# Kernel optimization log

Measured on AMD Instinct MI355X. Metric: run time of the kernel, lower is better.

The kernel has to match this reference:

```python
import jax, jax.numpy as jnp
import numpy as np

NUM_GRAPHS = 256
NODES_PER_GRAPH = 64
K = 24
HID = 128

elu = jax.nn.elu


def _knn_edge_conv(x, Wc, bc):
    # x: [B*N, D]. Recompute kNN graph per graph, edge MLP, max-aggregate.
    B, N = NUM_GRAPHS, NODES_PER_GRAPH
    xg = x.reshape(B, N, -1)                       # [B, N, D]
    sq = jnp.sum(xg * xg, axis=-1)                 # [B, N]
    # squared euclidean distances within each graph: [B, N, N]
    d = sq[:, :, None] + sq[:, None, :] - 2.0 * jnp.einsum('bnd,bmd->bnm', xg, xg)
    _, idx = jax.lax.top_k(-d, K)                  # [B, N, K] nearest (incl. self)
    xj = jax.vmap(lambda g, i: g[i])(xg, idx)      # [B, N, K, D] neighbor gather
    xi = xg[:, :, None, :]                         # [B, N, 1, D]
    e = jnp.concatenate([jnp.broadcast_to(xi, xj.shape), xj - xi], axis=-1)  # [B,N,K,2D]
    m = elu(jnp.einsum('bnkf,fh->bnkh', e, Wc) + bc)
    out = jnp.max(m, axis=2)                       # max aggregation over K neighbors
    return out.reshape(B * N, -1)


def setup_inputs() -> dict:
    key = jax.random.key(0)
    ks = jax.random.split(key, 16)
    Ntot = NUM_GRAPHS * NODES_PER_GRAPH

    def w(k, fan_in, fan_out):
        return jax.random.normal(k, (fan_in, fan_out), jnp.float32) / np.sqrt(fan_in)

    return {
        'x_pf': jax.random.normal(ks[0], (Ntot, 15), jnp.float32),
        'batch_pf': jnp.repeat(jnp.arange(NUM_GRAPHS, dtype=jnp.int64 if jax.config.jax_enable_x64 else jnp.int32), NODES_PER_GRAPH),
        'W1': w(ks[1], 15, HID),  'b1': jnp.zeros((HID,), jnp.float32),
        'W2': w(ks[2], HID, HID), 'b2': jnp.zeros((HID,), jnp.float32),
        'Wc': w(ks[3], 2 * HID, HID), 'bc': jnp.zeros((HID,), jnp.float32),
        'Wo1': w(ks[4], HID, 64), 'bo1': jnp.zeros((64,), jnp.float32),
        'Wo2': w(ks[5], 64, 32),  'bo2': jnp.zeros((32,), jnp.float32),
        'Wo3': w(ks[6], 32, 32),  'bo3': jnp.zeros((32,), jnp.float32),
        'Wo4': w(ks[7], 32, 8),   'bo4': jnp.zeros((8,), jnp.float32),
    }


def reference(x_pf, batch_pf, W1, b1, W2, b2, Wc, bc, Wo1, bo1, Wo2, bo2, Wo3, bo3, Wo4, bo4):
    # pf_encode: Linear(15,128)+ELU+Linear(128,128)+ELU
    h = elu(elu(x_pf @ W1 + b1) @ W2 + b2)
    f1 = _knn_edge_conv(h, Wc, bc)
    f2 = _knn_edge_conv(f1, Wc, bc)
    f3 = _knn_edge_conv(f2, Wc, bc)
    # global_add_pool over nodes per graph
    pooled = jax.ops.segment_sum(f3, batch_pf, num_segments=NUM_GRAPHS)  # [B, 128]
    o = elu(pooled @ Wo1 + bo1)
    o = elu(o @ Wo2 + bo2)
    o = elu(o @ Wo3 + bo3)
    out = o @ Wo4 + bo4  # [B, 8]
    return (out, batch_pf)
```

## Files before the change

### kernel.cpp

```cpp
#include <hip/hip_runtime.h>
#include <hip/hip_bf16.h>
#include <math.h>

#define NG  256
#define NN  64
#define KK  24
#define HID 128
#define KP  136
#define FP  132
#define DP  68
#define FRAG 512
#define SLAB (8*4*2*FRAG)
#define HSLAB (8*4*FRAG)
#define IMG_BYTES (3*SLAB*2)

typedef __attribute__((ext_vector_type(8)))  short bf16x8;
typedef __attribute__((ext_vector_type(4)))  float f32x4;

__device__ __forceinline__ float elu1(float x){ return x > 0.f ? x : (expf(x)-1.f); }

__device__ __forceinline__ short bf_t(float x){ return (short)(__float_as_uint(x) >> 16); }
__device__ __forceinline__ float bf_u(short s){ return __uint_as_float(((unsigned)(unsigned short)s) << 16); }

extern "C" __global__ void prep_kernel(const float* __restrict__ W2,
                                       const float* __restrict__ Wc,
                                       short* __restrict__ img)
{
    int t = blockIdx.x * 256 + threadIdx.x;
    if (t >= 3*8*4*64) return;
    const int lane = t & 63;
    const int ks   = (t >> 6) & 3;
    const int tn   = (t >> 8) & 7;
    const int s    = t >> 11;
    const int n     = tn*16 + (lane & 15);
    const int kbase = ks*32 + (lane >> 4)*8;
    bf16x8 hv, lv;
    #pragma unroll
    for (int j = 0; j < 8; ++j){
        const int k = kbase + j;
        float w = (s == 0) ? W2[k*HID + n]
                : (s == 1) ? Wc[k*HID + n]
                           : Wc[(k + HID)*HID + n];
        short h = bf_t(w);
        hv[j] = h;
        lv[j] = bf_t(w - bf_u(h));
    }
    short* dst = img + s*SLAB + ((tn*4 + ks)*2)*FRAG + lane*8;
    *(bf16x8*)(dst)        = hv;
    *(bf16x8*)(dst + FRAG) = lv;
}

__device__ __forceinline__ void stage_copy(const short* __restrict__ src,
                                           short* __restrict__ slab, int tid)
{
    const uint4* s = (const uint4*)src;
    uint4* d = (uint4*)slab;
    #pragma unroll
    for (int i = 0; i < 4; ++i) d[tid + i*1024] = s[tid + i*1024];
}

__device__ __forceinline__ void stage_build(const float* __restrict__ Wg, int rowoff,
                                            short* __restrict__ slab, int tid)
{
    for (int i = tid; i < 8*4*64; i += 1024){
        const int lane2 = i & 63;
        const int ks    = (i >> 6) & 3;
        const int tn    = (i >> 8) & 7;
        const int n     = tn*16 + (lane2 & 15);
        const int kbase = ks*32 + (lane2 >> 4)*8;
        bf16x8 hv, lv;
        #pragma unroll
        for (int j = 0; j < 8; ++j){
            float w = Wg[(rowoff + kbase + j)*HID + n];
            short h = bf_t(w);
            hv[j] = h;
            lv[j] = bf_t(w - bf_u(h));
        }
        short* dst = slab + ((tn*4 + ks)*2)*FRAG + lane2*8;
        *(bf16x8*)(dst)        = hv;
        *(bf16x8*)(dst + FRAG) = lv;
    }
}

__device__ __forceinline__ void stage_hi_uv(const short* __restrict__ img,
                                            short* __restrict__ uv, int tid)
{
    const uint4* s = (const uint4*)img;
    uint4* d = (uint4*)uv;
    #pragma unroll
    for (int k = 0; k < 4; ++k){
        const int idx    = tid + k*1024;
        const int sl     = idx >> 11;
        const int within = idx & 2047;
        const int f      = within >> 6;
        const int w      = within & 63;
        d[idx] = s[(1 + sl)*4096 + f*128 + w];
    }
}

__device__ __forceinline__ void build_hi_uv(const float* __restrict__ Wc,
                                            short* __restrict__ uv, int tid)
{
    #pragma unroll
    for (int k = 0; k < 4; ++k){
        const int idx    = tid + k*1024;
        const int sl     = idx >> 11;
        const int within = idx & 2047;
        const int f      = within >> 6;
        const int lane2  = within & 63;
        const int tn = f >> 2, ks = f & 3;
        const int n     = tn*16 + (lane2 & 15);
        const int kbase = ks*32 + (lane2 >> 4)*8;
        const int rowoff = sl ? HID : 0;
        bf16x8 hv;
        #pragma unroll
        for (int j = 0; j < 8; ++j) hv[j] = bf_t(Wc[(rowoff + kbase + j)*HID + n]);
        *(bf16x8*)(uv + (size_t)idx*8) = hv;
    }
}

__device__ __forceinline__ void gemm16x2(const short* __restrict__ fbhi,
                                         const short* __restrict__ fblo,
                                         const short* __restrict__ slab,
                                         int tm, int tn0, int tn1, int lane,
                                         f32x4& c0, f32x4& c1)
{
    const int arow = tm*16 + (lane & 15);
    const int ko   = (lane >> 4) * 8;
    #pragma unroll 2
    for (int ks = 0; ks < 4; ++ks){
        bf16x8 ah = *(const bf16x8*)(fbhi + arow*KP + ks*32 + ko);
        bf16x8 al = *(const bf16x8*)(fblo + arow*KP + ks*32 + ko);
        const short* p0 = slab + ((tn0*4 + ks)*2)*FRAG + lane*8;
        const short* p1 = slab + ((tn1*4 + ks)*2)*FRAG + lane*8;
        bf16x8 bh0 = *(const bf16x8*)(p0);
        bf16x8 bl0 = *(const bf16x8*)(p0 + FRAG);
        bf16x8 bh1 = *(const bf16x8*)(p1);
        bf16x8 bl1 = *(const bf16x8*)(p1 + FRAG);
        c0 = __builtin_amdgcn_mfma_f32_16x16x32_bf16(ah, bh0, c0, 0,0,0);
        c0 = __builtin_amdgcn_mfma_f32_16x16x32_bf16(ah, bl0, c0, 0,0,0);
        c0 = __builtin_amdgcn_mfma_f32_16x16x32_bf16(al, bh0, c0, 0,0,0);
        c1 = __builtin_amdgcn_mfma_f32_16x16x32_bf16(ah, bh1, c1, 0,0,0);
        c1 = __builtin_amdgcn_mfma_f32_16x16x32_bf16(ah, bl1, c1, 0,0,0);
        c1 = __builtin_amdgcn_mfma_f32_16x16x32_bf16(al, bh1, c1, 0,0,0);
    }
}

extern "C" __global__ void __launch_bounds__(1024)
dgcnn_kernel(const float* __restrict__ x_pf,
             const float* __restrict__ W1, const float* __restrict__ b1,
             const float* __restrict__ W2, const float* __restrict__ b2,
             const float* __restrict__ Wc, const float* __restrict__ bc,
             const float* __restrict__ Wo1, const float* __restrict__ bo1,
             const float* __restrict__ Wo2, const float* __restrict__ bo2,
             const float* __restrict__ Wo3, const float* __restrict__ bo3,
             const float* __restrict__ Wo4, const float* __restrict__ bo4,
             const short* __restrict__ img, int use_img,
             float* __restrict__ out)
{
    __shared__ __align__(16) short fbhi[NN*KP];
    __shared__ __align__(16) short fblo[NN*KP];
    __shared__ __align__(16) float dmt[NN*DP];
    __shared__ __align__(16) float Vbuf[NN*FP];
    __shared__ __align__(16) short wslab[SLAB];
    __shared__ int   knn[NN*KK];
    __shared__ float sq[NN];

    const int tid  = threadIdx.x;
    const int g    = blockIdx.x;
    const int lane = tid & 63;
    const int wv   = tid >> 6;
    const int row1 = tid >> 4;
    const int c0i  = (tid & 15) * 8;
    const int c2   = (tid & 15) * 4;

    const int t0  = wv*2, t1 = wv*2 + 1;
    const int gtm = t0 >> 3;
    const int gtn0 = t0 & 7, gtn1 = t1 & 7;

    if (tid < NN) out[NG*8 + g*NN + tid] = (float)g;

    if (use_img) stage_copy(img + 0*SLAB, wslab, tid); else stage_build(W2, 0, wslab, tid);

    {
        float acc[8];
        {
            float4 bA = *(const float4*)(b1 + c0i);
            float4 bB = *(const float4*)(b1 + c0i + 4);
            acc[0]=bA.x; acc[1]=bA.y; acc[2]=bA.z; acc[3]=bA.w;
            acc[4]=bB.x; acc[5]=bB.y; acc[6]=bB.z; acc[7]=bB.w;
        }
        #pragma unroll
        for (int f = 0; f < 15; ++f){
            float xv = x_pf[g*NN*15 + row1*15 + f];
            float4 wA = *(const float4*)(W1 + f*HID + c0i);
            float4 wB = *(const float4*)(W1 + f*HID + c0i + 4);
            acc[0] += xv*wA.x; acc[1] += xv*wA.y; acc[2] += xv*wA.z; acc[3] += xv*wA.w;
            acc[4] += xv*wB.x; acc[5] += xv*wB.y; acc[6] += xv*wB.z; acc[7] += xv*wB.w;
        }
        short4 hA, lA, hB, lB;
        float v;
        v = elu1(acc[0]); hA.x = bf_t(v); lA.x = bf_t(v - bf_u(hA.x));
        v = elu1(acc[1]); hA.y = bf_t(v); lA.y = bf_t(v - bf_u(hA.y));
        v = elu1(acc[2]); hA.z = bf_t(v); lA.z = bf_t(v - bf_u(hA.z));
        v = elu1(acc[3]); hA.w = bf_t(v); lA.w = bf_t(v - bf_u(hA.w));
        v = elu1(acc[4]); hB.x = bf_t(v); lB.x = bf_t(v - bf_u(hB.x));
        v = elu1(acc[5]); hB.y = bf_t(v); lB.y = bf_t(v - bf_u(hB.y));
        v = elu1(acc[6]); hB.z = bf_t(v); lB.z = bf_t(v - bf_u(hB.z));
        v = elu1(acc[7]); hB.w = bf_t(v); lB.w = bf_t(v - bf_u(hB.w));
        *(short4*)(fbhi + row1*KP + c0i)     = hA;
        *(short4*)(fbhi + row1*KP + c0i + 4) = hB;
        *(short4*)(fblo + row1*KP + c0i)     = lA;
        *(short4*)(fblo + row1*KP + c0i + 4) = lB;
    }
    __syncthreads();

    {
        f32x4 cA = {0,0,0,0}, cB = {0,0,0,0};
        gemm16x2(fbhi, fblo, wslab, gtm, gtn0, gtn1, lane, cA, cB);
        __syncthreads();
        #pragma unroll
        for (int half = 0; half < 2; ++half){
            const int tn  = half ? gtn1 : gtn0;
            const f32x4 c = half ? cB : cA;
            const int col = tn*16 + (lane & 15);
            const int rb  = gtm*16 + (lane >> 4)*4;
            const float bb = b2[col];
            #pragma unroll
            for (int e = 0; e < 4; ++e){
                float vv = elu1(c[e] + bb);
                short h = bf_t(vv);
                fbhi[(rb + e)*KP + col] = h;
                fblo[(rb + e)*KP + col] = bf_t(vv - bf_u(h));
            }
        }
        if (use_img) stage_hi_uv(img, wslab, tid); else build_hi_uv(Wc, wslab, tid);
    }
    __syncthreads();

    {
        bf16x8 hv = *(const bf16x8*)(fbhi + row1*KP + c0i);
        bf16x8 lv = *(const bf16x8*)(fblo + row1*KP + c0i);
        float s = 0.f;
        #pragma unroll
        for (int j = 0; j < 8; ++j){
            float vv = bf_u(hv[j]) + bf_u(lv[j]);
            s += vv*vv;
        }
        s += __shfl_xor(s, 1, 64);
        s += __shfl_xor(s, 2, 64);
        s += __shfl_xor(s, 4, 64);
        s += __shfl_xor(s, 8, 64);
        if ((tid & 15) == 0) sq[row1] = s;
    }
    __syncthreads();

    const short* Uhi = wslab;
    const short* Vhi = wslab + HSLAB;

    for (int layer = 0; layer < 3; ++layer){
        f32x4 uA = {0,0,0,0}, uB = {0,0,0,0}, vA = {0,0,0,0}, vB = {0,0,0,0};
        {
            f32x4 dc = {0.f, 0.f, 0.f, 0.f};
            const int tm0 = wv >> 2, tn0d = wv & 3;
            const int arow = tm0*16 + (lane & 15);
            const int rB   = tn0d*16 + (lane & 15);
            const int ko   = (lane >> 4) * 8;
            #pragma unroll
            for (int ks = 0; ks < 4; ++ks){
                bf16x8 ah = *(const bf16x8*)(fbhi + arow*KP + ks*32 + ko);
                bf16x8 al = *(const bf16x8*)(fblo + arow*KP + ks*32 + ko);
                bf16x8 bh = *(const bf16x8*)(fbhi + rB*KP + ks*32 + ko);
                bf16x8 bl = *(const bf16x8*)(fblo + rB*KP + ks*32 + ko);
                dc = __builtin_amdgcn_mfma_f32_16x16x32_bf16(ah, bh, dc, 0,0,0);
                dc = __builtin_amdgcn_mfma_f32_16x16x32_bf16(ah, bl, dc, 0,0,0);
                dc = __builtin_amdgcn_mfma_f32_16x16x32_bf16(al, bh, dc, 0,0,0);
                const int f0 = (gtn0*4 + ks)*FRAG + lane*8;
                const int f1 = (gtn1*4 + ks)*FRAG + lane*8;
                bf16x8 bu0 = *(const bf16x8*)(Uhi + f0);
                bf16x8 bu1 = *(const bf16x8*)(Uhi + f1);
                bf16x8 bv0 = *(const bf16x8*)(Vhi + f0);
                bf16x8 bv1 = *(const bf16x8*)(Vhi + f1);
                uA = __builtin_amdgcn_mfma_f32_16x16x32_bf16(ah, bu0, uA, 0,0,0);
                uA = __builtin_amdgcn_mfma_f32_16x16x32_bf16(al, bu0, uA, 0,0,0);
                uB = __builtin_amdgcn_mfma_f32_16x16x32_bf16(ah, bu1, uB, 0,0,0);
                uB = __builtin_amdgcn_mfma_f32_16x16x32_bf16(al, bu1, uB, 0,0,0);
                vA = __builtin_amdgcn_mfma_f32_16x16x32_bf16(ah, bv0, vA, 0,0,0);
                vA = __builtin_amdgcn_mfma_f32_16x16x32_bf16(al, bv0, vA, 0,0,0);
                vB = __builtin_amdgcn_mfma_f32_16x16x32_bf16(ah, bv1, vB, 0,0,0);
                vB = __builtin_amdgcn_mfma_f32_16x16x32_bf16(al, bv1, vB, 0,0,0);
            }
            #pragma unroll
            for (int e = 0; e < 4; ++e){
                const int ra = tm0*16 + (lane >> 4)*4 + e, ca = tn0d*16 + (lane & 15);
                dmt[ra*DP + ca] = sq[ra] + sq[ca] - 2.f*dc[e];
            }
        }
        __syncthreads();

        {
            #pragma unroll
            for (int half = 0; half < 2; ++half){
                const int tn  = half ? gtn1 : gtn0;
                const f32x4 cv = half ? vB : vA;
                const f32x4 cu = half ? uB : uA;
                const int col = tn*16 + (lane & 15);
                const int rb  = gtm*16 + (lane >> 4)*4;
                #pragma unroll
                for (int e = 0; e < 4; ++e){
                    Vbuf[(rb + e)*FP + col] = cv[e];
                    float u = cu[e];
                    short h = bf_t(u);
                    fbhi[(rb + e)*KP + col] = h;
                    fblo[(rb + e)*KP + col] = bf_t(u - bf_u(h));
                }
            }
            #pragma unroll
            for (int p = 0; p < 4; ++p){
                const int r = wv*4 + p;
                const float dm = dmt[r*DP + lane];
                int rank = 0;
                #pragma unroll 4
                for (int q = 0; q < 16; ++q){
                    float4 v = *(const float4*)(dmt + r*DP + q*4);
                    rank += (v.x < dm) + (v.y < dm) + (v.z < dm) + (v.w < dm);
                }
                const unsigned long long mask = __ballot(rank < KK);
                if (rank < KK){
                    const int c = __popcll(mask & ((1ULL << lane) - 1ULL));
                    if (c < KK) knn[r*KK + c] = lane;
                }
            }
        }
        __syncthreads();

        {
            const int* kr = knn + row1*KK;
            int4 j0 = *(const int4*)(kr);
            int4 j1 = *(const int4*)(kr + 4);
            int4 j2 = *(const int4*)(kr + 8);
            int4 j3 = *(const int4*)(kr + 12);
            int4 j4 = *(const int4*)(kr + 16);
            int4 j5 = *(const int4*)(kr + 20);
            float4 mxA = make_float4(-1e30f, -1e30f, -1e30f, -1e30f);
            float4 mxB = mxA;
            #define GM(J) { \
                float4 va = *(const float4*)(Vbuf + (J)*FP + c2); \
                float4 vb = *(const float4*)(Vbuf + (J)*FP + c2 + 64); \
                mxA.x = fmaxf(mxA.x, va.x); mxA.y = fmaxf(mxA.y, va.y); \
                mxA.z = fmaxf(mxA.z, va.z); mxA.w = fmaxf(mxA.w, va.w); \
                mxB.x = fmaxf(mxB.x, vb.x); mxB.y = fmaxf(mxB.y, vb.y); \
                mxB.z = fmaxf(mxB.z, vb.z); mxB.w = fmaxf(mxB.w, vb.w); }
            GM(j0.x) GM(j0.y) GM(j0.z) GM(j0.w)
            GM(j1.x) GM(j1.y) GM(j1.z) GM(j1.w)
            GM(j2.x) GM(j2.y) GM(j2.z) GM(j2.w)
            GM(j3.x) GM(j3.y) GM(j3.z) GM(j3.w)
            GM(j4.x) GM(j4.y) GM(j4.z) GM(j4.w)
            GM(j5.x) GM(j5.y) GM(j5.z) GM(j5.w)
            #undef GM
            float4 bcA = *(const float4*)(bc + c2);
            float4 bcB = *(const float4*)(bc + c2 + 64);
            float4 vnA = *(const float4*)(Vbuf + row1*FP + c2);
            float4 vnB = *(const float4*)(Vbuf + row1*FP + c2 + 64);
            short4 uhA = *(const short4*)(fbhi + row1*KP + c2);
            short4 uhB = *(const short4*)(fbhi + row1*KP + c2 + 64);
            short4 ulA = *(const short4*)(fblo + row1*KP + c2);
            short4 ulB = *(const short4*)(fblo + row1*KP + c2 + 64);
            float o0 = elu1(bf_u(uhA.x) + bf_u(ulA.x) - vnA.x + bcA.x + mxA.x);
            float o1 = elu1(bf_u(uhA.y) + bf_u(ulA.y) - vnA.y + bcA.y + mxA.y);
            float o2 = elu1(bf_u(uhA.z) + bf_u(ulA.z) - vnA.z + bcA.z + mxA.z);
            float o3 = elu1(bf_u(uhA.w) + bf_u(ulA.w) - vnA.w + bcA.w + mxA.w);
            float o4 = elu1(bf_u(uhB.x) + bf_u(ulB.x) - vnB.x + bcB.x + mxB.x);
            float o5 = elu1(bf_u(uhB.y) + bf_u(ulB.y) - vnB.y + bcB.y + mxB.y);
            float o6 = elu1(bf_u(uhB.z) + bf_u(ulB.z) - vnB.z + bcB.z + mxB.z);
            float o7 = elu1(bf_u(uhB.w) + bf_u(ulB.w) - vnB.w + bcB.w + mxB.w);
            short4 nhA, nlA, nhB, nlB;
            nhA.x = bf_t(o0); nlA.x = bf_t(o0 - bf_u(nhA.x));
            nhA.y = bf_t(o1); nlA.y = bf_t(o1 - bf_u(nhA.y));
            nhA.z = bf_t(o2); nlA.z = bf_t(o2 - bf_u(nhA.z));
            nhA.w = bf_t(o3); nlA.w = bf_t(o3 - bf_u(nhA.w));
            nhB.x = bf_t(o4); nlB.x = bf_t(o4 - bf_u(nhB.x));
            nhB.y = bf_t(o5); nlB.y = bf_t(o5 - bf_u(nhB.y));
            nhB.z = bf_t(o6); nlB.z = bf_t(o6 - bf_u(nhB.z));
            nhB.w = bf_t(o7); nlB.w = bf_t(o7 - bf_u(nhB.w));
            *(short4*)(fbhi + row1*KP + c2)      = nhA;
            *(short4*)(fbhi + row1*KP + c2 + 64) = nhB;
            *(short4*)(fblo + row1*KP + c2)      = nlA;
            *(short4*)(fblo + row1*KP + c2 + 64) = nlB;
            float s = o0*o0 + o1*o1 + o2*o2 + o3*o3 + o4*o4 + o5*o5 + o6*o6 + o7*o7;
            s += __shfl_xor(s, 1, 64);
            s += __shfl_xor(s, 2, 64);
            s += __shfl_xor(s, 4, 64);
            s += __shfl_xor(s, 8, 64);
            if ((tid & 15) == 0) sq[row1] = s;
        }
        __syncthreads();
    }

    float* pooled = Vbuf;
    float* red    = Vbuf + 128;
    float* hr1    = Vbuf + 1152;
    float* hr2    = Vbuf + 1216;
    float* hr3    = Vbuf + 1248;

    {
        const int pq = tid >> 7, ch = tid & 127;
        float s = 0.f;
        for (int n = pq*8; n < pq*8 + 8; ++n)
            s += bf_u(fbhi[n*KP + ch]) + bf_u(fblo[n*KP + ch]);
        red[pq*HID + ch] = s;
    }
    __syncthreads();
    if (tid < HID){
        float s = 0.f;
        #pragma unroll
        for (int p = 0; p < 8; ++p) s += red[p*HID + tid];
        pooled[tid] = s;
    }
    __syncthreads();
    if (tid < 256){
        const int o = tid & 63, part = tid >> 6;
        float s = 0.f;
        for (int f = part*32; f < part*32 + 32; ++f) s += pooled[f] * Wo1[f*64 + o];
        red[part*64 + o] = s;
    }
    __syncthreads();
    if (tid < 64) hr1[tid] = elu1(bo1[tid] + red[tid] + red[64+tid] + red[128+tid] + red[192+tid]);
    __syncthreads();
    if (tid < 128){
        const int o = tid & 31, part = tid >> 5;
        float s = 0.f;
        for (int f = part*16; f < part*16 + 16; ++f) s += hr1[f] * Wo2[f*32 + o];
        red[part*32 + o] = s;
    }
    __syncthreads();
    if (tid < 32) hr2[tid] = elu1(bo2[tid] + red[tid] + red[32+tid] + red[64+tid] + red[96+tid]);
    __syncthreads();
    if (tid < 32){
        float a = bo3[tid];
        for (int f = 0; f < 32; ++f) a += hr2[f] * Wo3[f*32 + tid];
        hr3[tid] = elu1(a);
    }
    __syncthreads();
    if (tid < 8){
        float a = bo4[tid];
        for (int f = 0; f < 32; ++f) a += hr3[f] * Wo4[f*8 + tid];
        out[g*8 + tid] = a;
    }
}

extern "C" void kernel_launch(void* const* d_in, const int* in_sizes, int n_in,
                              void* d_out, int out_size, void* d_ws, size_t ws_size,
                              hipStream_t stream) {
    short* img = (short*)d_ws;
    const int use_img = (ws_size >= (size_t)IMG_BYTES) ? 1 : 0;
    if (use_img) {
        const int total = 3*8*4*64;
        prep_kernel<<<(total + 255)/256, 256, 0, stream>>>(
            (const float*)d_in[4], (const float*)d_in[6], img);
    }
    dgcnn_kernel<<<NG, 1024, 0, stream>>>(
        (const float*)d_in[0],
        (const float*)d_in[2],  (const float*)d_in[3],
        (const float*)d_in[4],  (const float*)d_in[5],
        (const float*)d_in[6],  (const float*)d_in[7],
        (const float*)d_in[8],  (const float*)d_in[9],
        (const float*)d_in[10], (const float*)d_in[11],
        (const float*)d_in[12], (const float*)d_in[13],
        (const float*)d_in[14], (const float*)d_in[15],
        img, use_img,
        (float*)d_out);
}
```

Baseline: 52.51 us.

## Drop low-bf16 residual for U, use fast exp, byte-offset gathers, single-wave output MLP

Uses the fast __expf intrinsic in ELU and stores the U projection only as a single bf16 (high part), dropping the hi/lo split that kept it accurate. Neighbour indices are pre-scaled to byte offsets so each gather avoids an index multiply. The output MLP head now runs in a single wavefront with LDS waits in place of multiple block-wide __syncthreads. Precision of U and exp is lowered, which may affect accuracy and kNN tie ordering in later layers.

```diff
diff --git a/kernel.cpp b/kernel.cpp
--- a/kernel.cpp
+++ b/kernel.cpp
@@ -17,7 +17,7 @@
 typedef __attribute__((ext_vector_type(8)))  short bf16x8;
 typedef __attribute__((ext_vector_type(4)))  float f32x4;
 
-__device__ __forceinline__ float elu1(float x){ return x > 0.f ? x : (expf(x)-1.f); }
+__device__ __forceinline__ float elu1(float x){ return x > 0.f ? x : (__expf(x)-1.f); }
 
 __device__ __forceinline__ short bf_t(float x){ return (short)(__float_as_uint(x) >> 16); }
 __device__ __forceinline__ float bf_u(short s){ return __uint_as_float(((unsigned)(unsigned short)s) << 16); }
@@ -309,10 +309,7 @@
                 #pragma unroll
                 for (int e = 0; e < 4; ++e){
                     Vbuf[(rb + e)*FP + col] = cv[e];
-                    float u = cu[e];
-                    short h = bf_t(u);
-                    fbhi[(rb + e)*KP + col] = h;
-                    fblo[(rb + e)*KP + col] = bf_t(u - bf_u(h));
+                    fbhi[(rb + e)*KP + col] = bf_t(cu[e]);
                 }
             }
             #pragma unroll
@@ -328,7 +325,7 @@
                 const unsigned long long mask = __ballot(rank < KK);
                 if (rank < KK){
                     const int c = __popcll(mask & ((1ULL << lane) - 1ULL));
-                    if (c < KK) knn[r*KK + c] = lane;
+                    if (c < KK) knn[r*KK + c] = lane * (FP*4);
                 }
             }
         }
@@ -342,11 +339,12 @@
             int4 j3 = *(const int4*)(kr + 12);
             int4 j4 = *(const int4*)(kr + 16);
             int4 j5 = *(const int4*)(kr + 20);
+            const char* Vb = (const char*)Vbuf + c2*4;
             float4 mxA = make_float4(-1e30f, -1e30f, -1e30f, -1e30f);
             float4 mxB = mxA;
             #define GM(J) { \
-                float4 va = *(const float4*)(Vbuf + (J)*FP + c2); \
-                float4 vb = *(const float4*)(Vbuf + (J)*FP + c2 + 64); \
+                float4 va = *(const float4*)(Vb + (J)); \
+                float4 vb = *(const float4*)(Vb + (J) + 256); \
                 mxA.x = fmaxf(mxA.x, va.x); mxA.y = fmaxf(mxA.y, va.y); \
                 mxA.z = fmaxf(mxA.z, va.z); mxA.w = fmaxf(mxA.w, va.w); \
                 mxB.x = fmaxf(mxB.x, vb.x); mxB.y = fmaxf(mxB.y, vb.y); \
@@ -364,16 +362,14 @@
             float4 vnB = *(const float4*)(Vbuf + row1*FP + c2 + 64);
             short4 uhA = *(const short4*)(fbhi + row1*KP + c2);
             short4 uhB = *(const short4*)(fbhi + row1*KP + c2 + 64);
-            short4 ulA = *(const short4*)(fblo + row1*KP + c2);
-            short4 ulB = *(const short4*)(fblo + row1*KP + c2 + 64);
-            float o0 = elu1(bf_u(uhA.x) + bf_u(ulA.x) - vnA.x + bcA.x + mxA.x);
-            float o1 = elu1(bf_u(uhA.y) + bf_u(ulA.y) - vnA.y + bcA.y + mxA.y);
-            float o2 = elu1(bf_u(uhA.z) + bf_u(ulA.z) - vnA.z + bcA.z + mxA.z);
-            float o3 = elu1(bf_u(uhA.w) + bf_u(ulA.w) - vnA.w + bcA.w + mxA.w);
-            float o4 = elu1(bf_u(uhB.x) + bf_u(ulB.x) - vnB.x + bcB.x + mxB.x);
-            float o5 = elu1(bf_u(uhB.y) + bf_u(ulB.y) - vnB.y + bcB.y + mxB.y);
-            float o6 = elu1(bf_u(uhB.z) + bf_u(ulB.z) - vnB.z + bcB.z + mxB.z);
-            float o7 = elu1(bf_u(uhB.w) + bf_u(ulB.w) - vnB.w + bcB.w + mxB.w);
+            float o0 = elu1(bf_u(uhA.x) - vnA.x + bcA.x + mxA.x);
+            float o1 = elu1(bf_u(uhA.y) - vnA.y + bcA.y + mxA.y);
+            float o2 = elu1(bf_u(uhA.z) - vnA.z + bcA.z + mxA.z);
+            float o3 = elu1(bf_u(uhA.w) - vnA.w + bcA.w + mxA.w);
+            float o4 = elu1(bf_u(uhB.x) - vnB.x + bcB.x + mxB.x);
+            float o5 = elu1(bf_u(uhB.y) - vnB.y + bcB.y + mxB.y);
+            float o6 = elu1(bf_u(uhB.z) - vnB.z + bcB.z + mxB.z);
+            float o7 = elu1(bf_u(uhB.w) - vnB.w + bcB.w + mxB.w);
             short4 nhA, nlA, nhB, nlB;
             nhA.x = bf_t(o0); nlA.x = bf_t(o0 - bf_u(nhA.x));
             nhA.y = bf_t(o1); nlA.y = bf_t(o1 - bf_u(nhA.y));
@@ -418,34 +414,36 @@
         pooled[tid] = s;
     }
     __syncthreads();
-    if (tid < 256){
-        const int o = tid & 63, part = tid >> 6;
-        float s = 0.f;
-        for (int f = part*32; f < part*32 + 32; ++f) s += pooled[f] * Wo1[f*64 + o];
-        red[part*64 + o] = s;
-    }
-    __syncthreads();
-    if (tid < 64) hr1[tid] = elu1(bo1[tid] + red[tid] + red[64+tid] + red[128+tid] + red[192+tid]);
-    __syncthreads();
-    if (tid < 128){
-        const int o = tid & 31, part = tid >> 5;
-        float s = 0.f;
-        for (int f = part*16; f < part*16 + 16; ++f) s += hr1[f] * Wo2[f*32 + o];
-        red[part*32 + o] = s;
-    }
-    __syncthreads();
-    if (tid < 32) hr2[tid] = elu1(bo2[tid] + red[tid] + red[32+tid] + red[64+tid] + red[96+tid]);
-    __syncthreads();
-    if (tid < 32){
-        float a = bo3[tid];
-        for (int f = 0; f < 32; ++f) a += hr2[f] * Wo3[f*32 + tid];
-        hr3[tid] = elu1(a);
-    }
-    __syncthreads();
-    if (tid < 8){
-        float a = bo4[tid];
-        for (int f = 0; f < 32; ++f) a += hr3[f] * Wo4[f*8 + tid];
-        out[g*8 + tid] = a;
+
+    if (tid < 64){
+        float a1 = bo1[tid];
+        #pragma unroll 4
+        for (int f = 0; f < HID; ++f) a1 += pooled[f] * Wo1[f*64 + tid];
+        hr1[tid] = elu1(a1);
+        asm volatile("s_waitcnt lgkmcnt(0)" ::: "memory");
+        __builtin_amdgcn_sched_barrier(0);
+        if (tid < 32){
+            float a2 = bo2[tid];
+            #pragma unroll 4
+            for (int f = 0; f < 64; ++f) a2 += hr1[f] * Wo2[f*32 + tid];
+            hr2[tid] = elu1(a2);
+        }
+        asm volatile("s_waitcnt lgkmcnt(0)" ::: "memory");
+        __builtin_amdgcn_sched_barrier(0);
+        if (tid < 32){
+            float a3 = bo3[tid];
+            #pragma unroll 4
+            for (int f = 0; f < 32; ++f) a3 += hr2[f] * Wo3[f*32 + tid];
+            hr3[tid] = elu1(a3);
+        }
+        asm volatile("s_waitcnt lgkmcnt(0)" ::: "memory");
+        __builtin_amdgcn_sched_barrier(0);
+        if (tid < 8){
+            float a4 = bo4[tid];
+            #pragma unroll
+            for (int f = 0; f < 32; ++f) a4 += hr3[f] * Wo4[f*8 + tid];
+            out[g*8 + tid] = a4;
+        }
     }
 }
 
```

Measured after the change: 55.20 us. 1.05x slower.
